# Kernel optimization log

Measured on AMD Instinct MI355X. Metric: run time of the kernel, lower is better.

## Reference

```python
import jax, jax.numpy as jnp
import numpy as np


def conv1x1(x, w, b):
    # x: [B,C,H,W], w: [O,C], b: [O] -> [B,O,H,W]
    return jnp.einsum('bchw,oc->bohw', x, w) + b[None, :, None, None]


def setup_inputs() -> dict:
    key = jax.random.key(0)
    ks = jax.random.split(key, 8)
    B, C, H, W = 16, 256, 64, 64
    Cq = C // 8
    x = jax.random.normal(ks[0], (B, C, H, W), dtype=jnp.float32)
    wq = jax.random.normal(ks[1], (Cq, C), dtype=jnp.float32) * (2.0 / C) ** 0.5
    bq = jnp.zeros((Cq,), dtype=jnp.float32)
    wk = jax.random.normal(ks[2], (Cq, C), dtype=jnp.float32) * (2.0 / C) ** 0.5
    bk = jnp.zeros((Cq,), dtype=jnp.float32)
    wv = jax.random.normal(ks[3], (C, C), dtype=jnp.float32) * (2.0 / C) ** 0.5
    bv = jnp.zeros((C,), dtype=jnp.float32)
    gamma = jax.random.normal(ks[4], (1,), dtype=jnp.float32) * 0.1
    return {'x': x, 'wq': wq, 'bq': bq, 'wk': wk, 'bk': bk, 'wv': wv, 'bv': bv, 'gamma': gamma}


def reference(x, wq, bq, wk, bk, wv, bv, gamma):
    B, C, H, W = x.shape
    bH = B // 4
    bW = B // 4  # requires bH*bW == B, i.e. B == 16
    q = conv1x1(x, wq, bq)   # [B, C/8, H, W]
    k = conv1x1(x, wk, bk)   # [B, C/8, H, W]
    v = conv1x1(x, wv, bv)   # [B, C, H, W]
    # batch index b -> grid (h = b // bW, w = b % bW); token feature = flat map
    qg = q.reshape(bH, bW, -1)  # [bH, bW, Dq]
    kg = k.reshape(bH, bW, -1)
    vg = v.reshape(bH, bW, -1)  # [bH, bW, Dv]
    # column ('H') attention with -inf diagonal, row ('W') attention
    eH = jnp.einsum('hwd,gwd->hwg', qg, kg)  # [bH, bW, bH]
    eye = jnp.eye(bH, dtype=bool)[:, None, :]  # mask h == h'
    eH = jnp.where(eye, -jnp.inf, eH)
    eW = jnp.einsum('hwd,hgd->hwg', qg, kg)  # [bH, bW, bW]
    att = jax.nn.softmax(jnp.concatenate([eH, eW], axis=-1), axis=-1)
    aH, aW = att[..., :bH], att[..., bH:]
    oH = jnp.einsum('hwg,gwd->hwd', aH, vg)  # attend down the column
    oW = jnp.einsum('hwg,hgd->hwd', aW, vg)  # attend along the row
    out = (oH + oW).reshape(B, C, H, W)
    return gamma[0] * out + x
```

## Files before the change

kernel.cpp:

```cpp
#include <hip/hip_runtime.h>

#define B_   16
#define C_   256
#define HW_  4096
#define DQK  131072
#define DV   1048576

using bf16x8  = __attribute__((ext_vector_type(8))) __bf16;
using ushort8 = __attribute__((ext_vector_type(8))) unsigned short;
using u16x4   = __attribute__((ext_vector_type(4))) unsigned short;
using f32x4   = __attribute__((ext_vector_type(4))) float;

static __device__ __forceinline__ unsigned short f2bf(float f) {
    union { float f; unsigned u; } v; v.f = f;
    unsigned r = v.u + 0x7FFFu + ((v.u >> 16) & 1u);
    return (unsigned short)(r >> 16);
}
static __device__ __forceinline__ float bf2f(unsigned short h) {
    union { unsigned u; float f; } v; v.u = ((unsigned)h) << 16;
    return v.f;
}

__global__ __launch_bounds__(256) void k_pack(const float* wq, const float* wk, const float* wv,
                                              unsigned short* Wh, unsigned short* Wl, unsigned short* Wv) {
    int idx = blockIdx.x * 256 + threadIdx.x;
    if (idx < 16384) {
        float f = (idx < 8192) ? wq[idx] : wk[idx - 8192];
        unsigned short hi = f2bf(f);
        Wh[idx] = hi;
        Wl[idx] = f2bf(f - bf2f(hi));
    } else {
        int i = idx - 16384;
        Wv[i] = f2bf(wv[i]);
    }
}

__global__ __launch_bounds__(256) void k_gemm_qk(const unsigned short* __restrict__ Wh,
                                                 const unsigned short* __restrict__ Wl,
                                                 const float* __restrict__ x,
                                                 const float* __restrict__ bq, const float* __restrict__ bk,
                                                 float* __restrict__ QF, float* __restrict__ KF) {
    __shared__ __align__(16) unsigned short Ah[64][40], Al[64][40];
    __shared__ __align__(16) unsigned short Bh[128][40], Bl[128][40];
    int b  = blockIdx.y;
    int n0 = blockIdx.x * 128;
    int t = threadIdx.x;
    int lane = t & 63, wid = t >> 6;
    int wm = wid >> 1, wn = wid & 1;
    int lr = lane & 15, kg = lane >> 4;

    const float* xb = x + (size_t)b * DV;
    int am = t >> 2, akq = (t & 3) * 8;
    int bkr = t >> 3, bnq = (t & 7) * 16;

    f32x4 acc[2][4];
    for (int mi = 0; mi < 2; mi++)
        for (int ni = 0; ni < 4; ni++) acc[mi][ni] = (f32x4){0.f, 0.f, 0.f, 0.f};

    for (int kk = 0; kk < 8; kk++) {
        int k0 = kk * 32;
        *(ushort8*)&Ah[am][akq] = *(const ushort8*)(Wh + (size_t)am * 256 + k0 + akq);
        *(ushort8*)&Al[am][akq] = *(const ushort8*)(Wl + (size_t)am * 256 + k0 + akq);
        const float* srcb = xb + (size_t)(k0 + bkr) * HW_ + n0 + bnq;
        for (int e4 = 0; e4 < 4; e4++) {
            f32x4 v = *(const f32x4*)(srcb + e4 * 4);
            for (int e = 0; e < 4; e++) {
                float f = v[e];
                unsigned short hi = f2bf(f);
                Bh[bnq + e4 * 4 + e][bkr] = hi;
                Bl[bnq + e4 * 4 + e][bkr] = f2bf(f - bf2f(hi));
            }
        }
        __syncthreads();
        bf16x8 ah[2], al[2], bh[4], bl[4];
        for (int mi = 0; mi < 2; mi++) {
            ah[mi] = *(const bf16x8*)&Ah[wm * 32 + mi * 16 + lr][kg * 8];
            al[mi] = *(const bf16x8*)&Al[wm * 32 + mi * 16 + lr][kg * 8];
        }
        for (int ni = 0; ni < 4; ni++) {
            bh[ni] = *(const bf16x8*)&Bh[wn * 64 + ni * 16 + lr][kg * 8];
            bl[ni] = *(const bf16x8*)&Bl[wn * 64 + ni * 16 + lr][kg * 8];
        }
        for (int mi = 0; mi < 2; mi++)
            for (int ni = 0; ni < 4; ni++) {
                acc[mi][ni] = __builtin_amdgcn_mfma_f32_16x16x32_bf16(ah[mi], bh[ni], acc[mi][ni], 0, 0, 0);
                acc[mi][ni] = __builtin_amdgcn_mfma_f32_16x16x32_bf16(ah[mi], bl[ni], acc[mi][ni], 0, 0, 0);
                acc[mi][ni] = __builtin_amdgcn_mfma_f32_16x16x32_bf16(al[mi], bh[ni], acc[mi][ni], 0, 0, 0);
            }
        __syncthreads();
    }
    for (int mi = 0; mi < 2; mi++) {
        int mbase = wm * 32 + mi * 16 + kg * 4;
        for (int i = 0; i < 4; i++) {
            int m = mbase + i;
            float bias = (m < 32) ? bq[m] : bk[m - 32];
            for (int ni = 0; ni < 4; ni++) {
                int n = n0 + wn * 64 + ni * 16 + lr;
                float val = acc[mi][ni][i] + bias;
                if (m < 32) QF[(size_t)b * DQK + (size_t)m * HW_ + n] = val;
                else        KF[(size_t)b * DQK + (size_t)(m - 32) * HW_ + n] = val;
            }
        }
    }
}

__global__ __launch_bounds__(256) void k_scores_part(const float* __restrict__ QF, const float* __restrict__ KF,
                                                     float* __restrict__ Sp) {
    int bx = blockIdx.x;
    int p = bx >> 3, sl = bx & 7;
    int b = p >> 3, j = p & 7;
    int h = b >> 2, w = b & 3;
    int bp = (j < 4) ? (j * 4 + w) : (h * 4 + (j - 4));
    int t = threadIdx.x;
    const f32x4* Q4 = (const f32x4*)(QF + (size_t)b * DQK);
    const f32x4* K4 = (const f32x4*)(KF + (size_t)bp * DQK);
    float s = 0.f;
    for (int it = 0; it < 16; it++) {
        int i4 = sl * 4096 + it * 256 + t;
        f32x4 q = Q4[i4], k = K4[i4];
        s += q[0] * k[0] + q[1] * k[1] + q[2] * k[2] + q[3] * k[3];
    }
    for (int off = 32; off > 0; off >>= 1) s += __shfl_down(s, off);
    __shared__ float ws4[4];
    if ((t & 63) == 0) ws4[t >> 6] = s;
    __syncthreads();
    if (t == 0) Sp[bx] = ws4[0] + ws4[1] + ws4[2] + ws4[3];
}

__global__ void k_softmax(const float* __restrict__ Sp, const float* __restrict__ gamma,
                          float* __restrict__ Mm) {
    int t = threadIdx.x;
    if (t < 16) {
        int b = t, h = b >> 2, w = b & 3;
        float e[8];
        for (int j = 0; j < 8; j++) {
            float s = 0.f;
            for (int sl = 0; sl < 8; sl++) s += Sp[(b * 8 + j) * 8 + sl];
            e[j] = s;
        }
        e[h] = -INFINITY;
        float m = e[0];
        for (int j = 1; j < 8; j++) m = fmaxf(m, e[j]);
        float a[8], sum = 0.f;
        for (int j = 0; j < 8; j++) { a[j] = expf(e[j] - m); sum += a[j]; }
        float inv = 1.0f / sum;
        float g = gamma[0];
        float row[16];
        for (int c = 0; c < 16; c++) row[c] = 0.f;
        for (int gg = 0; gg < 4; gg++) if (gg != h) row[gg * 4 + w] += a[gg] * inv;
        for (int gg = 0; gg < 4; gg++) row[h * 4 + gg] += a[4 + gg] * inv;
        for (int c = 0; c < 16; c++) Mm[b * 16 + c] = row[c] * g;
        Mm[256 + b] = g;
    }
}

__global__ __launch_bounds__(256) void k_mix(const float* __restrict__ Mm, const float* __restrict__ x,
                                             unsigned short* __restrict__ Xm) {
    __shared__ float Ms[256];
    __shared__ unsigned short T[16][32][36];
    int t = threadIdx.x;
    int p0 = blockIdx.x * 32, c0 = blockIdx.y * 32;
    Ms[t] = Mm[t];

    int c_l = t >> 3, p4 = t & 7;
    f32x4 in4[16];
    for (int bp = 0; bp < 16; bp++)
        in4[bp] = *(const f32x4*)(x + (size_t)bp * DV + (size_t)(c0 + c_l) * HW_ + p0 + p4 * 4);
    __syncthreads();
    for (int b = 0; b < 16; b++) {
        f32x4 acc = (f32x4){0.f, 0.f, 0.f, 0.f};
        for (int bp = 0; bp < 16; bp++) {
            float wgt = Ms[b * 16 + bp];
            acc += wgt * in4[bp];
        }
        for (int e = 0; e < 4; e++) T[b][p4 * 4 + e][c_l] = f2bf(acc[e]);
    }
    __syncthreads();
    int p_l = t >> 3, cq = t & 7;
    for (int b = 0; b < 16; b++) {
        u16x4 v = *(const u16x4*)&T[b][p_l][cq * 4];
        *(u16x4*)(Xm + (size_t)b * DV + (size_t)(p0 + p_l) * C_ + c0 + cq * 4) = v;
    }
}

__global__ __launch_bounds__(256) void k_gemm_v_res(const unsigned short* __restrict__ Wv,
                                                    const unsigned short* __restrict__ Xm,
                                                    const float* __restrict__ bv,
                                                    const float* __restrict__ MmRs,
                                                    const float* __restrict__ x,
                                                    float* __restrict__ out) {
    __shared__ __align__(16) unsigned short As[64][40];
    __shared__ __align__(16) unsigned short Bs[128][40];
    int b  = blockIdx.z;
    int m0 = blockIdx.y * 64;
    int n0 = blockIdx.x * 128;
    int t = threadIdx.x;
    int lane = t & 63, wid = t >> 6;
    int wm = wid >> 1, wn = wid & 1;
    int lr = lane & 15, kg = lane >> 4;

    const unsigned short* xtb = Xm + (size_t)b * DV;
    int am = t >> 2, akq = (t & 3) * 8;
    int bn = t >> 1, bkh = (t & 1) * 16;

    f32x4 acc[2][4];
    for (int mi = 0; mi < 2; mi++)
        for (int ni = 0; ni < 4; ni++) acc[mi][ni] = (f32x4){0.f, 0.f, 0.f, 0.f};

    for (int kk = 0; kk < 8; kk++) {
        int k0 = kk * 32;
        *(ushort8*)&As[am][akq] = *(const ushort8*)(Wv + (size_t)(m0 + am) * 256 + k0 + akq);
        const unsigned short* src = xtb + (size_t)(n0 + bn) * C_ + k0 + bkh;
        *(ushort8*)&Bs[bn][bkh]     = *(const ushort8*)(src);
        *(ushort8*)&Bs[bn][bkh + 8] = *(const ushort8*)(src + 8);
        __syncthreads();
        bf16x8 a[2], bb[4];
        for (int mi = 0; mi < 2; mi++) a[mi]  = *(const bf16x8*)&As[wm * 32 + mi * 16 + lr][kg * 8];
        for (int ni = 0; ni < 4; ni++) bb[ni] = *(const bf16x8*)&Bs[wn * 64 + ni * 16 + lr][kg * 8];
        for (int mi = 0; mi < 2; mi++)
            for (int ni = 0; ni < 4; ni++)
                acc[mi][ni] = __builtin_amdgcn_mfma_f32_16x16x32_bf16(a[mi], bb[ni], acc[mi][ni], 0, 0, 0);
        __syncthreads();
    }
    float rs_b = MmRs[256 + b];
    for (int mi = 0; mi < 2; mi++) {
        int mbase = m0 + wm * 32 + mi * 16 + kg * 4;
        for (int i = 0; i < 4; i++) {
            int m = mbase + i;
            float bias = rs_b * bv[m];
            for (int ni = 0; ni < 4; ni++) {
                int n = n0 + wn * 64 + ni * 16 + lr;
                size_t idx = (size_t)b * DV + (size_t)m * HW_ + n;
                out[idx] = acc[mi][ni][i] + bias + x[idx];
            }
        }
    }
}

extern "C" void kernel_launch(void* const* d_in, const int* in_sizes, int n_in,
                              void* d_out, int out_size, void* d_ws, size_t ws_size,
                              hipStream_t stream) {
    (void)in_sizes; (void)n_in; (void)out_size; (void)ws_size;
    const float* x     = (const float*)d_in[0];
    const float* wq    = (const float*)d_in[1];
    const float* bq    = (const float*)d_in[2];
    const float* wk    = (const float*)d_in[3];
    const float* bk    = (const float*)d_in[4];
    const float* wv    = (const float*)d_in[5];
    const float* bv    = (const float*)d_in[6];
    const float* gamma = (const float*)d_in[7];

    char* ws = (char*)d_ws;
    unsigned short* Wh = (unsigned short*)(ws + 0);
    unsigned short* Wl = (unsigned short*)(ws + 32768);
    unsigned short* Wv = (unsigned short*)(ws + 65536);
    float*          QF = (float*)(ws + 196608);
    float*          KF = (float*)(ws + 8585216);
    unsigned short* Xm = (unsigned short*)(ws + 16973824);
    float*          Sp = (float*)(ws + 0);
    float*          Mm = (float*)(ws + 4096);
    float*          vo = (float*)d_out;

    k_pack       <<<320, 256, 0, stream>>>(wq, wk, wv, Wh, Wl, Wv);
    k_gemm_qk    <<<dim3(32, 16), 256, 0, stream>>>(Wh, Wl, x, bq, bk, QF, KF);
    k_scores_part<<<1024, 256, 0, stream>>>(QF, KF, Sp);
    k_softmax    <<<1, 64, 0, stream>>>(Sp, gamma, Mm);
    k_mix        <<<dim3(128, 8), 256, 0, stream>>>(Mm, x, Xm);
    k_gemm_v_res <<<dim3(32, 4, 16), 256, 0, stream>>>(Wv, Xm, bv, Mm, x, vo);
}
```

Baseline: 94.89 us.

## Swizzle QK smem, reuse Q/K across pairs in scores, chunk Xm layout

Adds an XOR swizzle to the B-tile shared-memory writes and reads in the QK GEMM to cut LDS bank conflicts from the transposed column stores. Rewrites the scores kernel so each block stages a slice of Q and K for all 16 batches in shared memory and computes all 128 pair dot products from it, instead of rereading Q/K from global memory once per pair. The softmax kernel now does the final reduction over 256 partial sums. Xm is re-laid out in 32-channel chunks, and the V GEMM uses a K-step of 64, halving barrier count at the cost of more shared memory.

```diff
diff --git a/kernel.cpp b/kernel.cpp
--- a/kernel.cpp
+++ b/kernel.cpp
@@ -52,6 +52,8 @@
     const float* xb = x + (size_t)b * DV;
     int am = t >> 2, akq = (t & 3) * 8;
     int bkr = t >> 3, bnq = (t & 7) * 16;
+    int swz_w = (t & 3) << 3;
+    int colw  = bkr ^ swz_w;
 
     f32x4 acc[2][4];
     for (int mi = 0; mi < 2; mi++)
@@ -67,8 +69,9 @@
             for (int e = 0; e < 4; e++) {
                 float f = v[e];
                 unsigned short hi = f2bf(f);
-                Bh[bnq + e4 * 4 + e][bkr] = hi;
-                Bl[bnq + e4 * 4 + e][bkr] = f2bf(f - bf2f(hi));
+                int row = bnq + e4 * 4 + e;
+                Bh[row][colw] = hi;
+                Bl[row][colw] = f2bf(f - bf2f(hi));
             }
         }
         __syncthreads();
@@ -78,8 +81,10 @@
             al[mi] = *(const bf16x8*)&Al[wm * 32 + mi * 16 + lr][kg * 8];
         }
         for (int ni = 0; ni < 4; ni++) {
-            bh[ni] = *(const bf16x8*)&Bh[wn * 64 + ni * 16 + lr][kg * 8];
-            bl[ni] = *(const bf16x8*)&Bl[wn * 64 + ni * 16 + lr][kg * 8];
+            int row = wn * 64 + ni * 16 + lr;
+            int cg  = (kg ^ ((wn * 4 + ni) & 3)) * 8;
+            bh[ni] = *(const bf16x8*)&Bh[row][cg];
+            bl[ni] = *(const bf16x8*)&Bl[row][cg];
         }
         for (int mi = 0; mi < 2; mi++)
             for (int ni = 0; ni < 4; ni++) {
@@ -104,51 +109,58 @@
     }
 }
 
-__global__ __launch_bounds__(256) void k_scores_part(const float* __restrict__ QF, const float* __restrict__ KF,
-                                                     float* __restrict__ Sp) {
-    int bx = blockIdx.x;
-    int p = bx >> 3, sl = bx & 7;
+__global__ __launch_bounds__(256) void k_scores2(const float* __restrict__ QF, const float* __restrict__ KF,
+                                                 float* __restrict__ Sp) {
+    __shared__ float Ql[16][520], Kl[16][520];
+    int s = blockIdx.x;
+    int m = s >> 3, off = (s & 7) * 512;
+    int t = threadIdx.x;
+    for (int b = 0; b < 16; b++) {
+        const float* qs = QF + (size_t)b * DQK + (size_t)m * HW_ + off;
+        const float* ks = KF + (size_t)b * DQK + (size_t)m * HW_ + off;
+        Ql[b][t]       = qs[t];
+        Ql[b][t + 256] = qs[t + 256];
+        Kl[b][t]       = ks[t];
+        Kl[b][t + 256] = ks[t + 256];
+    }
+    __syncthreads();
+    int p = t >> 1, h = t & 1;
     int b = p >> 3, j = p & 7;
-    int h = b >> 2, w = b & 3;
-    int bp = (j < 4) ? (j * 4 + w) : (h * 4 + (j - 4));
-    int t = threadIdx.x;
-    const f32x4* Q4 = (const f32x4*)(QF + (size_t)b * DQK);
-    const f32x4* K4 = (const f32x4*)(KF + (size_t)bp * DQK);
-    float s = 0.f;
-    for (int it = 0; it < 16; it++) {
-        int i4 = sl * 4096 + it * 256 + t;
-        f32x4 q = Q4[i4], k = K4[i4];
-        s += q[0] * k[0] + q[1] * k[1] + q[2] * k[2] + q[3] * k[3];
-    }
-    for (int off = 32; off > 0; off >>= 1) s += __shfl_down(s, off);
-    __shared__ float ws4[4];
-    if ((t & 63) == 0) ws4[t >> 6] = s;
-    __syncthreads();
-    if (t == 0) Sp[bx] = ws4[0] + ws4[1] + ws4[2] + ws4[3];
-}
-
-__global__ void k_softmax(const float* __restrict__ Sp, const float* __restrict__ gamma,
-                          float* __restrict__ Mm) {
-    int t = threadIdx.x;
+    int hb = b >> 2, wb = b & 3;
+    int bp = (j < 4) ? (j * 4 + wb) : (hb * 4 + (j - 4));
+    const f32x4* q4 = (const f32x4*)&Ql[b][h * 256];
+    const f32x4* k4 = (const f32x4*)&Kl[bp][h * 256];
+    f32x4 a4 = (f32x4){0.f, 0.f, 0.f, 0.f};
+    for (int i = 0; i < 64; i++) a4 += q4[i] * k4[i];
+    float sres = a4[0] + a4[1] + a4[2] + a4[3];
+    sres += __shfl_xor(sres, 1);
+    if (h == 0) Sp[(size_t)p * 256 + s] = sres;
+}
+
+__global__ void k_softmax2(const float* __restrict__ Sp, const float* __restrict__ gamma,
+                           float* __restrict__ Mm) {
+    __shared__ float SS[128];
+    int t = threadIdx.x;
+    const f32x4* s4 = (const f32x4*)(Sp + (size_t)t * 256);
+    f32x4 a = (f32x4){0.f, 0.f, 0.f, 0.f};
+    for (int i = 0; i < 64; i++) a += s4[i];
+    SS[t] = a[0] + a[1] + a[2] + a[3];
+    __syncthreads();
     if (t < 16) {
         int b = t, h = b >> 2, w = b & 3;
         float e[8];
-        for (int j = 0; j < 8; j++) {
-            float s = 0.f;
-            for (int sl = 0; sl < 8; sl++) s += Sp[(b * 8 + j) * 8 + sl];
-            e[j] = s;
-        }
+        for (int j = 0; j < 8; j++) e[j] = SS[b * 8 + j];
         e[h] = -INFINITY;
-        float m = e[0];
-        for (int j = 1; j < 8; j++) m = fmaxf(m, e[j]);
-        float a[8], sum = 0.f;
-        for (int j = 0; j < 8; j++) { a[j] = expf(e[j] - m); sum += a[j]; }
+        float mx = e[0];
+        for (int j = 1; j < 8; j++) mx = fmaxf(mx, e[j]);
+        float aa[8], sum = 0.f;
+        for (int j = 0; j < 8; j++) { aa[j] = expf(e[j] - mx); sum += aa[j]; }
         float inv = 1.0f / sum;
         float g = gamma[0];
         float row[16];
         for (int c = 0; c < 16; c++) row[c] = 0.f;
-        for (int gg = 0; gg < 4; gg++) if (gg != h) row[gg * 4 + w] += a[gg] * inv;
-        for (int gg = 0; gg < 4; gg++) row[h * 4 + gg] += a[4 + gg] * inv;
+        for (int gg = 0; gg < 4; gg++) if (gg != h) row[gg * 4 + w] += aa[gg] * inv;
+        for (int gg = 0; gg < 4; gg++) row[h * 4 + gg] += aa[4 + gg] * inv;
         for (int c = 0; c < 16; c++) Mm[b * 16 + c] = row[c] * g;
         Mm[256 + b] = g;
     }
@@ -159,7 +171,7 @@
     __shared__ float Ms[256];
     __shared__ unsigned short T[16][32][36];
     int t = threadIdx.x;
-    int p0 = blockIdx.x * 32, c0 = blockIdx.y * 32;
+    int p0 = blockIdx.x * 32, cb = blockIdx.y, c0 = cb * 32;
     Ms[t] = Mm[t];
 
     int c_l = t >> 3, p4 = t & 7;
@@ -179,7 +191,7 @@
     int p_l = t >> 3, cq = t & 7;
     for (int b = 0; b < 16; b++) {
         u16x4 v = *(const u16x4*)&T[b][p_l][cq * 4];
-        *(u16x4*)(Xm + (size_t)b * DV + (size_t)(p0 + p_l) * C_ + c0 + cq * 4) = v;
+        *(u16x4*)(Xm + ((size_t)(b * 8 + cb) * HW_ + p0 + p_l) * 32 + cq * 4) = v;
     }
 }
 
@@ -189,8 +201,8 @@
                                                     const float* __restrict__ MmRs,
                                                     const float* __restrict__ x,
                                                     float* __restrict__ out) {
-    __shared__ __align__(16) unsigned short As[64][40];
-    __shared__ __align__(16) unsigned short Bs[128][40];
+    __shared__ __align__(16) unsigned short As[64][72];
+    __shared__ __align__(16) unsigned short Bs[128][72];
     int b  = blockIdx.z;
     int m0 = blockIdx.y * 64;
     int n0 = blockIdx.x * 128;
@@ -199,27 +211,32 @@
     int wm = wid >> 1, wn = wid & 1;
     int lr = lane & 15, kg = lane >> 4;
 
-    const unsigned short* xtb = Xm + (size_t)b * DV;
-    int am = t >> 2, akq = (t & 3) * 8;
-    int bn = t >> 1, bkh = (t & 1) * 16;
+    int am = t >> 2, aq = (t & 3) * 16;
+    int bn = t >> 1, half = t & 1;
 
     f32x4 acc[2][4];
     for (int mi = 0; mi < 2; mi++)
         for (int ni = 0; ni < 4; ni++) acc[mi][ni] = (f32x4){0.f, 0.f, 0.f, 0.f};
 
-    for (int kk = 0; kk < 8; kk++) {
-        int k0 = kk * 32;
-        *(ushort8*)&As[am][akq] = *(const ushort8*)(Wv + (size_t)(m0 + am) * 256 + k0 + akq);
-        const unsigned short* src = xtb + (size_t)(n0 + bn) * C_ + k0 + bkh;
-        *(ushort8*)&Bs[bn][bkh]     = *(const ushort8*)(src);
-        *(ushort8*)&Bs[bn][bkh + 8] = *(const ushort8*)(src + 8);
-        __syncthreads();
-        bf16x8 a[2], bb[4];
-        for (int mi = 0; mi < 2; mi++) a[mi]  = *(const bf16x8*)&As[wm * 32 + mi * 16 + lr][kg * 8];
-        for (int ni = 0; ni < 4; ni++) bb[ni] = *(const bf16x8*)&Bs[wn * 64 + ni * 16 + lr][kg * 8];
-        for (int mi = 0; mi < 2; mi++)
-            for (int ni = 0; ni < 4; ni++)
-                acc[mi][ni] = __builtin_amdgcn_mfma_f32_16x16x32_bf16(a[mi], bb[ni], acc[mi][ni], 0, 0, 0);
+    for (int kk = 0; kk < 4; kk++) {
+        int k0 = kk * 64;
+        *(ushort8*)&As[am][aq]     = *(const ushort8*)(Wv + (size_t)(m0 + am) * 256 + k0 + aq);
+        *(ushort8*)&As[am][aq + 8] = *(const ushort8*)(Wv + (size_t)(m0 + am) * 256 + k0 + aq + 8);
+        const unsigned short* c0p = Xm + ((size_t)(b * 8 + kk * 2)     * HW_ + n0 + bn) * 32 + half * 16;
+        const unsigned short* c1p = Xm + ((size_t)(b * 8 + kk * 2 + 1) * HW_ + n0 + bn) * 32 + half * 16;
+        *(ushort8*)&Bs[bn][half * 16]          = *(const ushort8*)(c0p);
+        *(ushort8*)&Bs[bn][half * 16 + 8]      = *(const ushort8*)(c0p + 8);
+        *(ushort8*)&Bs[bn][32 + half * 16]     = *(const ushort8*)(c1p);
+        *(ushort8*)&Bs[bn][32 + half * 16 + 8] = *(const ushort8*)(c1p + 8);
+        __syncthreads();
+        for (int ks = 0; ks < 2; ks++) {
+            bf16x8 a[2], bb[4];
+            for (int mi = 0; mi < 2; mi++) a[mi]  = *(const bf16x8*)&As[wm * 32 + mi * 16 + lr][ks * 32 + kg * 8];
+            for (int ni = 0; ni < 4; ni++) bb[ni] = *(const bf16x8*)&Bs[wn * 64 + ni * 16 + lr][ks * 32 + kg * 8];
+            for (int mi = 0; mi < 2; mi++)
+                for (int ni = 0; ni < 4; ni++)
+                    acc[mi][ni] = __builtin_amdgcn_mfma_f32_16x16x32_bf16(a[mi], bb[ni], acc[mi][ni], 0, 0, 0);
+        }
         __syncthreads();
     }
     float rs_b = MmRs[256 + b];
@@ -257,14 +274,14 @@
     float*          QF = (float*)(ws + 196608);
     float*          KF = (float*)(ws + 8585216);
     unsigned short* Xm = (unsigned short*)(ws + 16973824);
-    float*          Sp = (float*)(ws + 0);
-    float*          Mm = (float*)(ws + 4096);
+    float*          Sp = (float*)(ws + 16973824);
+    float*          Mm = (float*)(ws + 0);
     float*          vo = (float*)d_out;
 
     k_pack       <<<320, 256, 0, stream>>>(wq, wk, wv, Wh, Wl, Wv);
     k_gemm_qk    <<<dim3(32, 16), 256, 0, stream>>>(Wh, Wl, x, bq, bk, QF, KF);
-    k_scores_part<<<1024, 256, 0, stream>>>(QF, KF, Sp);
-    k_softmax    <<<1, 64, 0, stream>>>(Sp, gamma, Mm);
+    k_scores2    <<<256, 256, 0, stream>>>(QF, KF, Sp);
+    k_softmax2   <<<1, 128, 0, stream>>>(Sp, gamma, Mm);
     k_mix        <<<dim3(128, 8), 256, 0, stream>>>(Mm, x, Xm);
     k_gemm_v_res <<<dim3(32, 4, 16), 256, 0, stream>>>(Wv, Xm, bv, Mm, x, vo);
 }
```

Measured after the change: 99.79 us. 1.05x slower.
